# Kernel tuning notes

Hardware: AMD Instinct MI355X
Metric: run time of the kernel (lower is better)

Reference implementation:

```python
import jax, jax.numpy as jnp
import numpy as np

B, T, C, H = 4, 2048, 768, 12
HS = C // H

def setup_inputs() -> dict:
    key = jax.random.key(0)
    ks = jax.random.split(key, 5)
    s = 0.02
    return {
        "x": jax.random.normal(ks[0], (B, T, C), jnp.float32),
        "W_attn": jax.random.normal(ks[1], (C, 3 * C), jnp.float32) * s,
        "b_attn": jnp.zeros((3 * C,), jnp.float32),
        "W_proj": jax.random.normal(ks[2], (C, C), jnp.float32) * s,
        "b_proj": jnp.zeros((C,), jnp.float32),
    }

def reference(x, W_attn, b_attn, W_proj, b_proj):
    Bz, Tz, Cz = x.shape
    qkv = x @ W_attn + b_attn                       # [B,T,3C]
    q, k, v = jnp.split(qkv, 3, axis=-1)
    # [B,T,C] -> [B,H,T,HS]
    def heads(t):
        return t.reshape(Bz, Tz, H, HS).transpose(0, 2, 1, 3)
    q, k, v = heads(q), heads(k), heads(v)
    scale = 1.0 / jnp.sqrt(jnp.asarray(HS, x.dtype))
    att = jnp.einsum("bhqd,bhkd->bhqk", q, k) * scale  # [B,H,T,T]
    causal = jnp.tril(jnp.ones((Tz, Tz), bool))
    att = jnp.where(causal[None, None], att, -jnp.inf)
    att = jax.nn.softmax(att, axis=-1)
    y = jnp.einsum("bhqk,bhkd->bhqd", att, v)       # [B,H,T,HS]
    y = y.transpose(0, 2, 1, 3).reshape(Bz, Tz, Cz)
    return y @ W_proj + b_proj
```

## Files before the change

### kernel.cpp

```cpp
#include <hip/hip_runtime.h>
#include <hip/hip_bf16.h>


typedef short s16x8 __attribute__((ext_vector_type(8)));
typedef float f32x4 __attribute__((ext_vector_type(4)));
typedef unsigned short u16x4 __attribute__((ext_vector_type(4)));
typedef unsigned short u16x8 __attribute__((ext_vector_type(8)));

#define MFMA16 __builtin_amdgcn_mfma_f32_16x16x32_bf16

__device__ __forceinline__ unsigned short f2bf(float f) {
    union { float f; unsigned u; } v; v.f = f;
    unsigned r = v.u + 0x7FFFu + ((v.u >> 16) & 1u);
    return (unsigned short)(r >> 16);
}

__device__ __forceinline__ void gload16(const unsigned short* g, unsigned short* l) {
    __builtin_amdgcn_global_load_lds(
        (__attribute__((address_space(1))) void*)(const void*)g,
        (__attribute__((address_space(3))) void*)l, 16, 0, 0);
}

__global__ __launch_bounds__(256) void cvt_f32_bf16(
    const float* __restrict__ src, unsigned short* __restrict__ dst, int n4)
{
    int i = blockIdx.x * 256 + threadIdx.x;
    if (i >= n4) return;
    float4 v = reinterpret_cast<const float4*>(src)[i];
    u16x4 o = { f2bf(v.x), f2bf(v.y), f2bf(v.z), f2bf(v.w) };
    reinterpret_cast<u16x4*>(dst)[i] = o;
}

__global__ __launch_bounds__(256) void cvt_transpose(
    const float* __restrict__ src, unsigned short* __restrict__ dst, int R, int C)
{
    __shared__ unsigned short tile[32][33];
    const int c0 = blockIdx.x * 32, r0 = blockIdx.y * 32;
    const int tx = threadIdx.x & 31, ty = threadIdx.x >> 5;
#pragma unroll
    for (int j = 0; j < 32; j += 8)
        tile[ty + j][tx] = f2bf(src[(size_t)(r0 + ty + j) * C + c0 + tx]);
    __syncthreads();
#pragma unroll
    for (int j = 0; j < 32; j += 8)
        dst[(size_t)(c0 + ty + j) * R + r0 + tx] = tile[tx][ty + j];
}

template<bool SCALEQ, bool OUT_BF16>
__global__ __launch_bounds__(256, 2) void gemm_bt(
    const unsigned short* __restrict__ A, const unsigned short* __restrict__ Bt,
    const float* __restrict__ bias, void* __restrict__ Cout,
    int M, int N, int K)
{
    __shared__ unsigned short lds_a[128 * 32];
    __shared__ unsigned short lds_b[128 * 32];

    const int tid = threadIdx.x, lane = tid & 63, w = tid >> 6;
    const int wr = w >> 1, wc = w & 1;
    const int m0 = blockIdx.y * 128, n0 = blockIdx.x * 128;
    const int lr = lane & 15, lg = lane >> 4;

    f32x4 acc[4][4];
#pragma unroll
    for (int mi = 0; mi < 4; ++mi)
#pragma unroll
        for (int ni = 0; ni < 4; ++ni)
            acc[mi][ni] = f32x4{0.f, 0.f, 0.f, 0.f};

    const int sr = tid >> 2, sc = (tid & 3) * 8;
    const unsigned short* Ap = A  + (size_t)(m0 + sr) * K + sc;
    const unsigned short* Aq = A  + (size_t)(m0 + 64 + sr) * K + sc;
    const unsigned short* Bp = Bt + (size_t)(n0 + sr) * K + sc;
    const unsigned short* Bq = Bt + (size_t)(n0 + 64 + sr) * K + sc;
    unsigned short* la0 = lds_a + (w << 9);
    unsigned short* la1 = lds_a + 2048 + (w << 9);
    unsigned short* lb0 = lds_b + (w << 9);
    unsigned short* lb1 = lds_b + 2048 + (w << 9);

    for (int k0 = 0; k0 < K; k0 += 32) {
        gload16(Ap + k0, la0);
        gload16(Aq + k0, la1);
        gload16(Bp + k0, lb0);
        gload16(Bq + k0, lb1);
        __syncthreads();

        s16x8 af[4], bfr[4];
#pragma unroll
        for (int mi = 0; mi < 4; ++mi)
            af[mi] = *reinterpret_cast<const s16x8*>(&lds_a[(wr * 64 + mi * 16 + lr) * 32 + lg * 8]);
#pragma unroll
        for (int ni = 0; ni < 4; ++ni)
            bfr[ni] = *reinterpret_cast<const s16x8*>(&lds_b[(wc * 64 + ni * 16 + lr) * 32 + lg * 8]);
#pragma unroll
        for (int mi = 0; mi < 4; ++mi)
#pragma unroll
            for (int ni = 0; ni < 4; ++ni)
                acc[mi][ni] = MFMA16(af[mi], bfr[ni], acc[mi][ni], 0, 0, 0);
        __syncthreads();
    }

#pragma unroll
    for (int ni = 0; ni < 4; ++ni) {
        int col = n0 + wc * 64 + ni * 16 + lr;
        float bs = bias[col];
        float scq = (SCALEQ && col < 768) ? 0.18033688011112042f : 1.0f;
#pragma unroll
        for (int mi = 0; mi < 4; ++mi)
#pragma unroll
            for (int r = 0; r < 4; ++r) {
                int row = m0 + wr * 64 + mi * 16 + lg * 4 + r;
                float v = (acc[mi][ni][r] + bs) * scq;
                if (OUT_BF16)
                    ((unsigned short*)Cout)[(size_t)row * N + col] = f2bf(v);
                else
                    ((float*)Cout)[(size_t)row * N + col] = v;
            }
    }
}

__global__ __launch_bounds__(256, 4) void attn_fwd(
    const unsigned short* __restrict__ qkv, unsigned short* __restrict__ att)
{
    __shared__ unsigned short lds_k[64 * 72];
    __shared__ unsigned short lds_v[64 * 72 + 64];
    __shared__ unsigned short lds_p[4][32 * 72];

    const int tid = threadIdx.x, lane = tid & 63, w = tid >> 6;
    const int lr = lane & 15, lg = lane >> 4;
    const int bh = blockIdx.x;
    const int qt = 15 - blockIdx.y;
    const int b = bh / 12, h = bh % 12;
    const size_t bT = (size_t)b * 2048;
    const int q0 = qt * 128;
    const int wq = q0 + w * 32;

    s16x8 qf[2][2];
#pragma unroll
    for (int mi = 0; mi < 2; ++mi) {
        const size_t qoff = (bT + wq + mi * 16 + lr) * 2304 + h * 64 + lg * 8;
        qf[mi][0] = *reinterpret_cast<const s16x8*>(qkv + qoff);
        qf[mi][1] = *reinterpret_cast<const s16x8*>(qkv + qoff + 32);
    }

    f32x4 o[2][4];
    f32x4 lsum[2];
#pragma unroll
    for (int mi = 0; mi < 2; ++mi) {
        lsum[mi] = f32x4{0.f, 0.f, 0.f, 0.f};
#pragma unroll
        for (int dt = 0; dt < 4; ++dt) o[mi][dt] = f32x4{0.f, 0.f, 0.f, 0.f};
    }

    const int sr = tid >> 2, sc = (tid & 3) * 16;
    const unsigned short* kbase = qkv + (bT + sr) * 2304 + 768 + h * 64 + sc;
    const unsigned short* vbase = qkv + (bT + sr) * 2304 + 1536 + h * 64 + sc;
    unsigned short* kdst = &lds_k[sr * 72 + sc];
    unsigned short* vdst = &lds_v[sc * 72 + ((sc >> 3) & 7) * 8 + sr];
    const int lrx = lr ^ ((lg & 1) << 3);
    const int nb16 = ((lg >> 1) & 1) << 4;
    const int rsel = ((lr >> 2) & 3) << 3;

    const int nkt = 2 * (qt + 1);

    u16x8 kr0, kr1, vr0, vr1;
    kr0 = *reinterpret_cast<const u16x8*>(kbase);
    kr1 = *reinterpret_cast<const u16x8*>(kbase + 8);
    vr0 = *reinterpret_cast<const u16x8*>(vbase);
    vr1 = *reinterpret_cast<const u16x8*>(vbase + 8);

    for (int kt = 0; kt < nkt; ++kt) {
        const int kv0 = kt * 64;
        *reinterpret_cast<u16x8*>(kdst)     = kr0;
        *reinterpret_cast<u16x8*>(kdst + 8) = kr1;
#pragma unroll
        for (int jj = 0; jj < 8; ++jj)
            vdst[jj * 72 + (jj >> 3) * 8] = vr0[jj];
#pragma unroll
        for (int jj = 8; jj < 16; ++jj)
            vdst[jj * 72 + (jj >> 3) * 8] = vr1[jj - 8];
        __syncthreads();

        {
            const int ktn = (kt + 1 < nkt) ? kt + 1 : kt;
            const size_t off = (size_t)(ktn * 64) * 2304;
            kr0 = *reinterpret_cast<const u16x8*>(kbase + off);
            kr1 = *reinterpret_cast<const u16x8*>(kbase + off + 8);
            vr0 = *reinterpret_cast<const u16x8*>(vbase + off);
            vr1 = *reinterpret_cast<const u16x8*>(vbase + off + 8);
        }

        if (kv0 <= wq + 31) {
            f32x4 sf[2][4];
#pragma unroll
            for (int mi = 0; mi < 2; ++mi)
#pragma unroll
                for (int n = 0; n < 4; ++n) sf[mi][n] = f32x4{0.f, 0.f, 0.f, 0.f};
#pragma unroll
            for (int kk = 0; kk < 2; ++kk)
#pragma unroll
                for (int n = 0; n < 4; ++n) {
                    s16x8 kf = *reinterpret_cast<const s16x8*>(&lds_k[(n * 16 + lr) * 72 + kk * 32 + lg * 8]);
                    sf[0][n] = MFMA16(qf[0][kk], kf, sf[0][n], 0, 0, 0);
                    sf[1][n] = MFMA16(qf[1][kk], kf, sf[1][n], 0, 0, 0);
                }

            if (kv0 + 63 > wq) {
#pragma unroll
                for (int mi = 0; mi < 2; ++mi)
#pragma unroll
                    for (int n = 0; n < 4; ++n)
#pragma unroll
                        for (int r = 0; r < 4; ++r) {
                            int key = kv0 + n * 16 + lr;
                            int row = wq + mi * 16 + lg * 4 + r;
                            if (key > row) sf[mi][n][r] = -1.0e30f;
                        }
            }

#pragma unroll
            for (int mi = 0; mi < 2; ++mi)
#pragma unroll
                for (int n = 0; n < 4; ++n) {
                    f32x4 p;
#pragma unroll
                    for (int r = 0; r < 4; ++r) p[r] = __builtin_amdgcn_exp2f(sf[mi][n][r]);
                    lsum[mi] += p;
                    const int kx = ((n << 4) ^ nb16) + lrx;
#pragma unroll
                    for (int r = 0; r < 4; ++r)
                        lds_p[w][(mi * 16 + lg * 4 + r) * 72 + kx] = f2bf(p[r]);
                }

#pragma unroll
            for (int kk = 0; kk < 2; ++kk) {
                const int pko = (kk * 32 + lg * 8) ^ rsel;
                s16x8 pf0 = *reinterpret_cast<const s16x8*>(&lds_p[w][lr * 72 + pko]);
                s16x8 pf1 = *reinterpret_cast<const s16x8*>(&lds_p[w][(16 + lr) * 72 + pko]);
#pragma unroll
                for (int dt = 0; dt < 4; ++dt) {
                    const int vrow = dt * 16 + lr;
                    s16x8 vf = *reinterpret_cast<const s16x8*>(
                        &lds_v[vrow * 72 + ((vrow >> 3) & 7) * 8 + kk * 32 + lg * 8]);
                    o[0][dt] = MFMA16(pf0, vf, o[0][dt], 0, 0, 0);
                    o[1][dt] = MFMA16(pf1, vf, o[1][dt], 0, 0, 0);
                }
            }
        }
        __syncthreads();
    }

#pragma unroll
    for (int mi = 0; mi < 2; ++mi)
#pragma unroll
        for (int mask = 1; mask < 16; mask <<= 1)
#pragma unroll
            for (int r = 0; r < 4; ++r)
                lsum[mi][r] += __shfl_xor(lsum[mi][r], mask);

#pragma unroll
    for (int mi = 0; mi < 2; ++mi)
#pragma unroll
        for (int dt = 0; dt < 4; ++dt)
#pragma unroll
            for (int r = 0; r < 4; ++r) {
                int row = wq + mi * 16 + lg * 4 + r;
                att[(bT + row) * 768 + h * 64 + dt * 16 + lr] = f2bf(o[mi][dt][r] / lsum[mi][r]);
            }
}

extern "C" void kernel_launch(void* const* d_in, const int* in_sizes, int n_in,
                              void* d_out, int out_size, void* d_ws, size_t ws_size,
                              hipStream_t stream) {
    const float* x      = (const float*)d_in[0];
    const float* W_attn = (const float*)d_in[1];
    const float* b_attn = (const float*)d_in[2];
    const float* W_proj = (const float*)d_in[3];
    const float* b_proj = (const float*)d_in[4];

    unsigned short* ws    = (unsigned short*)d_ws;
    unsigned short* x_bf  = ws;
    unsigned short* wa_t  = x_bf + 6291456;
    unsigned short* wp_t  = wa_t + 1769472;
    unsigned short* qkv   = wp_t + 589824;
    unsigned short* att   = qkv + 18874368;

    cvt_f32_bf16<<<6144, 256, 0, stream>>>(x, x_bf, 6291456 / 4);
    cvt_transpose<<<dim3(72, 24), 256, 0, stream>>>(W_attn, wa_t, 768, 2304);
    cvt_transpose<<<dim3(24, 24), 256, 0, stream>>>(W_proj, wp_t, 768, 768);

    gemm_bt<true , true ><<<dim3(18, 64), 256, 0, stream>>>(x_bf, wa_t, b_attn, qkv, 8192, 2304, 768);
    attn_fwd<<<dim3(48, 16), 256, 0, stream>>>(qkv, att);
    gemm_bt<false, false><<<dim3(6, 64), 256, 0, stream>>>(att, wp_t, b_proj, d_out, 8192, 768, 768);
}
```

Before: 223.2 us.

## Deepen GEMM K-tile to 64 with swizzled LDS, block remap, and 64-wide proj GEMM

```diff
diff --git a/kernel.cpp b/kernel.cpp
--- a/kernel.cpp
+++ b/kernel.cpp
@@ -10,9 +10,8 @@
 #define MFMA16 __builtin_amdgcn_mfma_f32_16x16x32_bf16
 
 __device__ __forceinline__ unsigned short f2bf(float f) {
-    union { float f; unsigned u; } v; v.f = f;
-    unsigned r = v.u + 0x7FFFu + ((v.u >> 16) & 1u);
-    return (unsigned short)(r >> 16);
+    __hip_bfloat16 h = __float2bfloat16(f);
+    return *reinterpret_cast<unsigned short*>(&h);
 }
 
 __device__ __forceinline__ void gload16(const unsigned short* g, unsigned short* l) {
@@ -52,13 +51,18 @@
     const float* __restrict__ bias, void* __restrict__ Cout,
     int M, int N, int K)
 {
-    __shared__ unsigned short lds_a[128 * 32];
-    __shared__ unsigned short lds_b[128 * 32];
+    __shared__ unsigned short lds_a[128 * 64];
+    __shared__ unsigned short lds_b[128 * 64];
 
     const int tid = threadIdx.x, lane = tid & 63, w = tid >> 6;
     const int wr = w >> 1, wc = w & 1;
-    const int m0 = blockIdx.y * 128, n0 = blockIdx.x * 128;
     const int lr = lane & 15, lg = lane >> 4;
+
+    const int nbx = gridDim.x;
+    const int bid = blockIdx.x + nbx * blockIdx.y;
+    const int cpx = (nbx * gridDim.y) >> 3;
+    const int swz = (bid & 7) * cpx + (bid >> 3);
+    const int m0 = (swz / nbx) * 128, n0 = (swz % nbx) * 128;
 
     f32x4 acc[4][4];
 #pragma unroll
@@ -67,35 +71,42 @@
         for (int ni = 0; ni < 4; ++ni)
             acc[mi][ni] = f32x4{0.f, 0.f, 0.f, 0.f};
 
-    const int sr = tid >> 2, sc = (tid & 3) * 8;
-    const unsigned short* Ap = A  + (size_t)(m0 + sr) * K + sc;
-    const unsigned short* Aq = A  + (size_t)(m0 + 64 + sr) * K + sc;
-    const unsigned short* Bp = Bt + (size_t)(n0 + sr) * K + sc;
-    const unsigned short* Bq = Bt + (size_t)(n0 + 64 + sr) * K + sc;
-    unsigned short* la0 = lds_a + (w << 9);
-    unsigned short* la1 = lds_a + 2048 + (w << 9);
-    unsigned short* lb0 = lds_b + (w << 9);
-    unsigned short* lb1 = lds_b + 2048 + (w << 9);
-
-    for (int k0 = 0; k0 < K; k0 += 32) {
-        gload16(Ap + k0, la0);
-        gload16(Aq + k0, la1);
-        gload16(Bp + k0, lb0);
-        gload16(Bq + k0, lb1);
-        __syncthreads();
-
-        s16x8 af[4], bfr[4];
-#pragma unroll
-        for (int mi = 0; mi < 4; ++mi)
-            af[mi] = *reinterpret_cast<const s16x8*>(&lds_a[(wr * 64 + mi * 16 + lr) * 32 + lg * 8]);
-#pragma unroll
-        for (int ni = 0; ni < 4; ++ni)
-            bfr[ni] = *reinterpret_cast<const s16x8*>(&lds_b[(wc * 64 + ni * 16 + lr) * 32 + lg * 8]);
-#pragma unroll
-        for (int mi = 0; mi < 4; ++mi)
-#pragma unroll
-            for (int ni = 0; ni < 4; ++ni)
-                acc[mi][ni] = MFMA16(af[mi], bfr[ni], acc[mi][ni], 0, 0, 0);
+    const int srow = 8 * w + (lane >> 3);
+    const int sslot = ((lane & 7) ^ (lane >> 3)) * 8;
+    const unsigned short* Ap = A  + (size_t)(m0 + srow) * K + sslot;
+    const unsigned short* Bp = Bt + (size_t)(n0 + srow) * K + sslot;
+    unsigned short* la = lds_a + w * 512;
+    unsigned short* lb = lds_b + w * 512;
+
+    for (int k0 = 0; k0 < K; k0 += 64) {
+#pragma unroll
+        for (int p = 0; p < 4; ++p) {
+            gload16(Ap + (size_t)(32 * p) * K + k0, la + 2048 * p);
+            gload16(Bp + (size_t)(32 * p) * K + k0, lb + 2048 * p);
+        }
+        __syncthreads();
+
+#pragma unroll
+        for (int kh = 0; kh < 2; ++kh) {
+            s16x8 af[4], bfr[4];
+#pragma unroll
+            for (int mi = 0; mi < 4; ++mi) {
+                const int row = wr * 64 + mi * 16 + lr;
+                af[mi] = *reinterpret_cast<const s16x8*>(
+                    &lds_a[row * 64 + ((kh * 32 + lg * 8) ^ ((row & 7) << 3))]);
+            }
+#pragma unroll
+            for (int ni = 0; ni < 4; ++ni) {
+                const int row = wc * 64 + ni * 16 + lr;
+                bfr[ni] = *reinterpret_cast<const s16x8*>(
+                    &lds_b[row * 64 + ((kh * 32 + lg * 8) ^ ((row & 7) << 3))]);
+            }
+#pragma unroll
+            for (int mi = 0; mi < 4; ++mi)
+#pragma unroll
+                for (int ni = 0; ni < 4; ++ni)
+                    acc[mi][ni] = MFMA16(af[mi], bfr[ni], acc[mi][ni], 0, 0, 0);
+        }
         __syncthreads();
     }
 
@@ -114,6 +125,84 @@
                     ((unsigned short*)Cout)[(size_t)row * N + col] = f2bf(v);
                 else
                     ((float*)Cout)[(size_t)row * N + col] = v;
+            }
+    }
+}
+
+__global__ __launch_bounds__(256, 3) void gemm_bt64(
+    const unsigned short* __restrict__ A, const unsigned short* __restrict__ Bt,
+    const float* __restrict__ bias, float* __restrict__ Cout,
+    int M, int N, int K)
+{
+    __shared__ unsigned short lds_a[128 * 64];
+    __shared__ unsigned short lds_b[64 * 64];
+
+    const int tid = threadIdx.x, lane = tid & 63, w = tid >> 6;
+    const int lr = lane & 15, lg = lane >> 4;
+
+    const int nbx = gridDim.x;
+    const int bid = blockIdx.x + nbx * blockIdx.y;
+    const int cpx = (nbx * gridDim.y) >> 3;
+    const int swz = (bid & 7) * cpx + (bid >> 3);
+    const int m0 = (swz / nbx) * 128, n0 = (swz % nbx) * 64;
+
+    f32x4 acc[2][4];
+#pragma unroll
+    for (int mi = 0; mi < 2; ++mi)
+#pragma unroll
+        for (int ni = 0; ni < 4; ++ni)
+            acc[mi][ni] = f32x4{0.f, 0.f, 0.f, 0.f};
+
+    const int srow = 8 * w + (lane >> 3);
+    const int sslot = ((lane & 7) ^ (lane >> 3)) * 8;
+    const unsigned short* Ap = A  + (size_t)(m0 + srow) * K + sslot;
+    const unsigned short* Bp = Bt + (size_t)(n0 + srow) * K + sslot;
+    unsigned short* la = lds_a + w * 512;
+    unsigned short* lb = lds_b + w * 512;
+
+    for (int k0 = 0; k0 < K; k0 += 64) {
+#pragma unroll
+        for (int p = 0; p < 4; ++p)
+            gload16(Ap + (size_t)(32 * p) * K + k0, la + 2048 * p);
+#pragma unroll
+        for (int p = 0; p < 2; ++p)
+            gload16(Bp + (size_t)(32 * p) * K + k0, lb + 2048 * p);
+        __syncthreads();
+
+#pragma unroll
+        for (int kh = 0; kh < 2; ++kh) {
+            s16x8 af[2], bfr[4];
+#pragma unroll
+            for (int mi = 0; mi < 2; ++mi) {
+                const int row = w * 32 + mi * 16 + lr;
+                af[mi] = *reinterpret_cast<const s16x8*>(
+                    &lds_a[row * 64 + ((kh * 32 + lg * 8) ^ ((row & 7) << 3))]);
+            }
+#pragma unroll
+            for (int ni = 0; ni < 4; ++ni) {
+                const int row = ni * 16 + lr;
+                bfr[ni] = *reinterpret_cast<const s16x8*>(
+                    &lds_b[row * 64 + ((kh * 32 + lg * 8) ^ ((row & 7) << 3))]);
+            }
+#pragma unroll
+            for (int mi = 0; mi < 2; ++mi)
+#pragma unroll
+                for (int ni = 0; ni < 4; ++ni)
+                    acc[mi][ni] = MFMA16(af[mi], bfr[ni], acc[mi][ni], 0, 0, 0);
+        }
+        __syncthreads();
+    }
+
+#pragma unroll
+    for (int ni = 0; ni < 4; ++ni) {
+        int col = n0 + ni * 16 + lr;
+        float bs = bias[col];
+#pragma unroll
+        for (int mi = 0; mi < 2; ++mi)
+#pragma unroll
+            for (int r = 0; r < 4; ++r) {
+                int row = m0 + w * 32 + mi * 16 + lg * 4 + r;
+                Cout[(size_t)row * N + col] = acc[mi][ni][r] + bs;
             }
     }
 }
@@ -263,8 +352,8 @@
         for (int dt = 0; dt < 4; ++dt)
 #pragma unroll
             for (int r = 0; r < 4; ++r) {
-                int row = wq + mi * 16 + lg * 4 + r;
-                att[(bT + row) * 768 + h * 64 + dt * 16 + lr] = f2bf(o[mi][dt][r] / lsum[mi][r]);
+                int qrow = wq + mi * 16 + lg * 4 + r;
+                att[(bT + qrow) * 768 + h * 64 + dt * 16 + lr] = f2bf(o[mi][dt][r] / lsum[mi][r]);
             }
 }
 
@@ -290,5 +379,5 @@
 
     gemm_bt<true , true ><<<dim3(18, 64), 256, 0, stream>>>(x_bf, wa_t, b_attn, qkv, 8192, 2304, 768);
     attn_fwd<<<dim3(48, 16), 256, 0, stream>>>(qkv, att);
-    gemm_bt<false, false><<<dim3(6, 64), 256, 0, stream>>>(att, wp_t, b_proj, d_out, 8192, 768, 768);
-}
+    gemm_bt64<<<dim3(12, 64), 256, 0, stream>>>(att, wp_t, b_proj, (float*)d_out, 8192, 768, 768);
+}
```

Result: faster. 207.8 us (-6.9%).
